# Optimization experiments

Measured on AMD Instinct MI355X. Metric: run time of the kernel, lower is better.

Reference implementation:

```python
import jax, jax.numpy as jnp
import numpy as np

NUM_ENT = 50000
DIM = 128
NUM_REL = 1000  # num_rel * 2 (inverse relations)
E = 300000
SLOPE = 0.2      # args.leaky_relu_w
BN_EPS = 1e-5


def _leaky(x):
    return jax.nn.leaky_relu(x, SLOPE)


def _l2norm(x):
    n = jnp.linalg.norm(x, axis=-1, keepdims=True)
    return x / jnp.maximum(n, 1e-12)


def _batchnorm(x):
    # BatchNorm1d, training mode, fresh gamma=1/beta=0
    m = x.mean(axis=0)
    v = x.var(axis=0)
    return (x - m) / jnp.sqrt(v + BN_EPS)


def _propagate(i, j, etype, rel, x, watt, aatt, gcn, norm, num_ent):
    # gather -> relation-aware transform (opn='mult') -> attention -> scatter-add
    trans = x[j] * rel[etype]                       # [E, D]
    comb = jnp.concatenate([x[i], trans], axis=1)   # [E, 2D]
    score = (_leaky(comb @ watt) @ aatt)[:, 0]      # [E]
    # scatter softmax of attention score over destination nodes
    m = jax.ops.segment_max(score, i, num_segments=num_ent)
    m = jnp.where(jnp.isfinite(m), m, 0.0)
    e = jnp.exp(score - m[i])
    s = jax.ops.segment_sum(e, i, num_segments=num_ent)
    alpha = e / (s[i] + 1e-16)
    msg = (trans @ gcn) * alpha[:, None]
    if norm is not None:
        msg = msg * norm[:, None]
    return jax.ops.segment_sum(msg, i, num_segments=num_ent)


def _conv(ent, rel_in, edge_index, edge_type, w1, w2, gcn, loop_rel, watt, aatt):
    # RelationalAwareLayer.forward
    num_ent = ent.shape[0]
    rel = jnp.concatenate([rel_in, loop_rel], axis=0)
    rel = _leaky(rel @ w1) @ w2
    row, col = edge_index[0], edge_index[1]
    deg = jax.ops.segment_sum(jnp.ones((row.shape[0],), jnp.float32), row, num_segments=num_ent)
    dinv = jnp.where(deg > 0, deg ** -0.5, 0.0)
    norm = dinv[row]
    msg_n = _propagate(row, col, edge_type, rel, ent, watt, aatt, gcn, norm, num_ent)
    idx = jnp.arange(num_ent)
    loop_t = jnp.full((num_ent,), rel.shape[0] - 1)
    msg_s = _propagate(idx, idx, loop_t, rel, ent, watt, aatt, gcn, None, num_ent)
    return jnp.tanh(_batchnorm((msg_n + msg_s) / 2.0))


def setup_inputs() -> dict:
    key = jax.random.key(0)
    ks = jax.random.split(key, 24)
    g = lambda k, s: jax.random.normal(k, s, dtype=jnp.float32) * 0.05
    return {
        'edge_index': jax.random.randint(ks[0], (2, E), 0, NUM_ENT),
        'edge_type': jax.random.randint(ks[1], (E,), 0, NUM_REL),
        'ent_info_att': g(ks[2], (NUM_ENT, DIM)),
        'ent_completion_att': g(ks[3], (NUM_ENT, DIM)),
        'rel_completion_att': g(ks[4], (NUM_REL, DIM)),
        'rel_info_att': g(ks[5], (NUM_REL, DIM)),
        'align_linear1_1': g(ks[6], (2 * DIM, DIM)),
        'align_linear1_2': g(ks[7], (DIM, DIM)),
        'align_linear2_1': g(ks[8], (2 * DIM, DIM)),
        'align_linear2_2': g(ks[9], (DIM, DIM)),
        'rel_linear11': g(ks[10], (DIM, DIM)),
        'rel_linear12': g(ks[11], (DIM, DIM)),
        'rel_linear11_align': g(ks[12], (DIM, DIM)),
        'rel_linear12_align': g(ks[13], (DIM, DIM)),
        'all_linear_comp': g(ks[14], (3 * DIM, DIM)),
        # stacked per-layer conv params: [conv1_align, conv1_completion, conv2_align]
        'conv_w1': g(ks[15], (3, DIM, DIM)),
        'conv_w2': g(ks[16], (3, DIM, DIM)),
        'conv_gcn': g(ks[17], (3, DIM, DIM)),
        'conv_loop': g(ks[18], (3, 1, DIM)),
        'conv_watt': g(ks[19], (3, 2 * DIM, DIM)),
        'conv_aatt': g(ks[20], (3, DIM, 1)),
    }


def reference(edge_index, edge_type, ent_info_att, ent_completion_att,
              rel_completion_att, rel_info_att,
              align_linear1_1, align_linear1_2, align_linear2_1, align_linear2_2,
              rel_linear11, rel_linear12, rel_linear11_align, rel_linear12_align,
              all_linear_comp, conv_w1, conv_w2, conv_gcn, conv_loop, conv_watt, conv_aatt):
    # forward_base with num_gcn_layer == 2, dropout rate 0 (identity)
    init_comp = _l2norm(ent_completion_att)
    e1 = _leaky(jnp.concatenate([init_comp, ent_info_att], axis=1) @ align_linear1_1) @ align_linear1_2
    ao1 = _conv(e1, rel_info_att, edge_index, edge_type,
                conv_w1[0], conv_w2[0], conv_gcn[0], conv_loop[0], conv_watt[0], conv_aatt[0])
    co1 = _conv(ent_completion_att, rel_completion_att, edge_index, edge_type,
                conv_w1[1], conv_w2[1], conv_gcn[1], conv_loop[1], conv_watt[1], conv_aatt[1])
    pos1n = _l2norm(co1)
    e2 = _leaky(jnp.concatenate([pos1n, ao1], axis=1) @ align_linear2_1) @ align_linear2_2
    pr1 = _leaky(rel_completion_att @ rel_linear11) @ rel_linear12
    ari = _leaky(rel_info_att @ rel_linear11_align) @ rel_linear12_align
    ao2 = _conv(e2, ari, edge_index, edge_type,
                conv_w1[2], conv_w2[2], conv_gcn[2], conv_loop[2], conv_watt[2], conv_aatt[2])
    out = jnp.concatenate([e1, ao1, ao2], axis=1) @ all_linear_comp
    return (out, co1, pr1)
```

## Files before the change

### kernel.cpp

```cpp
#include <hip/hip_runtime.h>
#include <hip/hip_bf16.h>
#include <math.h>

#define D 128
#define DD 16384
#define NEMAX 96
typedef unsigned short u16;
typedef __attribute__((ext_vector_type(8))) short short8v;
typedef __attribute__((ext_vector_type(4))) short short4v;
typedef __attribute__((ext_vector_type(4))) float f32x4;

__device__ __forceinline__ u16 f2s(float v){
    union { __hip_bfloat16 h; u16 u; } c; c.h = __float2bfloat16(v); return c.u;
}
__device__ __forceinline__ float s2f(u16 u){
    union { __hip_bfloat16 h; u16 u; } c; c.u = u; return __bfloat162float(c.h);
}
__device__ __forceinline__ float lrelu(float x){ return x > 0.f ? x : 0.2f*x; }

__global__ void k_prepz(int* __restrict__ zz, int zw, int* __restrict__ nstart,
                        int* __restrict__ nend, int nb){
    int i = blockIdx.x*blockDim.x + threadIdx.x;
    int stride = gridDim.x*blockDim.x;
    for (int k = i; k < zw; k += stride) zz[k] = 0;
    for (int k = i; k < nb; k += stride){ nstart[k] = 0x7fffffff; nend[k] = -1; }
}
__global__ void k_f2b4(const float* __restrict__ in, u16* __restrict__ out, int n4){
    for (int i = blockIdx.x*blockDim.x + threadIdx.x; i < n4; i += gridDim.x*blockDim.x){
        float4 a = ((const float4*)in)[i];
        short4v pk;
        pk[0] = (short)f2s(a.x); pk[1] = (short)f2s(a.y);
        pk[2] = (short)f2s(a.z); pk[3] = (short)f2s(a.w);
        *(short4v*)(out + (size_t)i*4) = pk;
    }
}
__global__ void k_ideg(const int* __restrict__ row, int* __restrict__ deg, int E_){
    for (int i = blockIdx.x*blockDim.x + threadIdx.x; i < E_; i += gridDim.x*blockDim.x)
        atomicAdd(&deg[row[i]], 1);
}
__global__ void k_scan1(const int* __restrict__ ideg, int* __restrict__ rowptr,
                        int* __restrict__ bsum, int n){
    __shared__ int buf[256];
    int t = threadIdx.x, i = blockIdx.x*256 + t;
    int v = (i < n) ? ideg[i] : 0;
    buf[t] = v;
    __syncthreads();
    #pragma unroll
    for (int o = 1; o < 256; o <<= 1){
        int u = (t >= o) ? buf[t-o] : 0;
        __syncthreads();
        buf[t] += u;
        __syncthreads();
    }
    if (i < n) rowptr[i] = buf[t] - v;
    if (t == 255) bsum[blockIdx.x] = buf[255];
}
__global__ void k_scan2(int* __restrict__ bsum, int nb){
    __shared__ int buf[256];
    __shared__ int carry_s;
    int t = threadIdx.x;
    if (t == 0) carry_s = 0;
    __syncthreads();
    for (int base = 0; base < nb; base += 256){
        int v = (base + t < nb) ? bsum[base + t] : 0;
        buf[t] = v;
        __syncthreads();
        #pragma unroll
        for (int o = 1; o < 256; o <<= 1){
            int u = (t >= o) ? buf[t-o] : 0;
            __syncthreads();
            buf[t] += u;
            __syncthreads();
        }
        if (base + t < nb) bsum[base + t] = carry_s + buf[t] - v;
        int last = buf[255];
        __syncthreads();
        if (t == 0) carry_s += last;
        __syncthreads();
    }
}
__global__ void k_scan3(int* __restrict__ rowptr, const int* __restrict__ bsum,
                        int n, int E_){
    int i = blockIdx.x*blockDim.x + threadIdx.x;
    if (i < n) rowptr[i] += bsum[i >> 8];
    if (i == 0) rowptr[n] = E_;
}
__global__ void k_scatter(const int* __restrict__ row, const int* __restrict__ rowptr,
                          int* __restrict__ cnt, int* __restrict__ perm, int E_){
    for (int e = blockIdx.x*blockDim.x + threadIdx.x; e < E_; e += gridDim.x*blockDim.x){
        int i = row[e];
        int pos = rowptr[i] + atomicAdd(&cnt[i], 1);
        perm[pos] = e;
    }
}
__global__ void k_bmap(const int* __restrict__ rowptr, int* __restrict__ nstart,
                       int* __restrict__ nend, int n){
    for (int i = blockIdx.x*blockDim.x + threadIdx.x; i < n; i += gridDim.x*blockDim.x){
        int s = rowptr[i], e = rowptr[i+1];
        if (e > s){
            int b = s >> 6;
            atomicMin(&nstart[b], i);
            atomicMax(&nend[b], i);
        }
    }
}
__global__ void k_bnapply(const float* __restrict__ acc, const float* __restrict__ gp,
                          float inv_ne, int n, u16* __restrict__ dstb,
                          float* __restrict__ dstf){
    int d = threadIdx.x & 127;
    float m = gp[d] * inv_ne;
    float var = gp[128 + d] * inv_ne - m*m;
    float sc = rsqrtf(var + 1e-5f);
    for (int i = blockIdx.x*blockDim.x + threadIdx.x; i < n; i += gridDim.x*blockDim.x){
        float v = acc[i] * 0.5f;
        float r = tanhf((v - m) * sc);
        dstb[i] = f2s(r);
        if (dstf) dstf[i] = r;
    }
}

__global__ void k_relprep(const float* __restrict__ rel_comp, const float* __restrict__ rel_info,
        const float* __restrict__ rl11, const float* __restrict__ rl12,
        const float* __restrict__ rl11a, const float* __restrict__ rl12a,
        const float* __restrict__ cloop, const float* __restrict__ cw1,
        const float* __restrict__ cw2, float* __restrict__ pr1out,
        float* __restrict__ rel2all, int NR){
    int b = blockIdx.x, t = threadIdx.x;
    __shared__ float v[D];
    __shared__ float h[D];
    if (b < NR){
        v[t] = rel_comp[(size_t)b*D + t];
        __syncthreads();
        float a = 0.f;
        #pragma unroll 8
        for (int k = 0; k < D; k++) a += v[k] * rl11[(size_t)k*D + t];
        h[t] = lrelu(a);
        __syncthreads();
        float o = 0.f;
        #pragma unroll 8
        for (int k = 0; k < D; k++) o += h[k] * rl12[(size_t)k*D + t];
        pr1out[(size_t)b*D + t] = o;
        return;
    }
    int bb = b - NR;
    int l = bb / (NR+1), r = bb - l*(NR+1);
    float xv;
    if (r == NR)      xv = cloop[l*D + t];
    else if (l == 1)  xv = rel_comp[(size_t)r*D + t];
    else              xv = rel_info[(size_t)r*D + t];
    v[t] = xv;
    __syncthreads();
    if (l == 2 && r < NR){
        float a = 0.f;
        #pragma unroll 8
        for (int k = 0; k < D; k++) a += v[k] * rl11a[(size_t)k*D + t];
        h[t] = lrelu(a);
        __syncthreads();
        float o = 0.f;
        #pragma unroll 8
        for (int k = 0; k < D; k++) o += h[k] * rl12a[(size_t)k*D + t];
        v[t] = o;
        __syncthreads();
    }
    const float* w1 = cw1 + (size_t)l*DD;
    const float* w2 = cw2 + (size_t)l*DD;
    float a = 0.f;
    #pragma unroll 8
    for (int k = 0; k < D; k++) a += v[k] * w1[(size_t)k*D + t];
    h[t] = lrelu(a);
    __syncthreads();
    float o = 0.f;
    #pragma unroll 8
    for (int k = 0; k < D; k++) o += h[k] * w2[(size_t)k*D + t];
    rel2all[((size_t)l*(NR+1) + r)*D + t] = o;
}

struct TEnt { const float* s; u16* d; int ldd; };
struct TTab { TEnt e[18]; };
__global__ void k_wprep(TTab tab){
    TEnt en = tab.e[blockIdx.x];
    int t = threadIdx.x;
    int n = t >> 1, h = t & 1;
    #pragma unroll
    for (int g = 0; g < 8; ++g){
        int k0 = h*64 + g*8;
        short8v pk;
        #pragma unroll
        for (int q = 0; q < 8; ++q) pk[q] = (short)f2s(en.s[(size_t)(k0+q)*D + n]);
        *(short8v*)(en.d + (size_t)n*en.ldd + k0) = pk;
    }
}

struct Srcs { const void* p0; const void* p1; const void* p2; int f0, f1, f2; };

template<int NSEG, int EPI, bool RSN>
__global__ __launch_bounds__(256) void k_mrow(Srcs S, const u16* __restrict__ WT,
        void* __restrict__ out, int NE_, float* __restrict__ gp,
        u16* __restrict__ uout, const float* __restrict__ looprow){
    __shared__ __align__(16) short As[128*128];
    int tid = threadIdx.x;
    int row0 = blockIdx.x * 128;
    int lane = tid & 63, w = tid >> 6;
    int l15 = lane & 15, lq = lane >> 4;
    int nhalf = w & 1, mquad = w >> 1;
    f32x4 acc[4][4];
    #pragma unroll
    for (int a = 0; a < 4; a++)
        #pragma unroll
        for (int b = 0; b < 4; b++) acc[a][b] = (f32x4){0.f,0.f,0.f,0.f};

    int sr = tid >> 1, sh = tid & 1;
    int rr = row0 + sr; if (rr >= NE_) rr = NE_ - 1;

    #pragma unroll
    for (int s = 0; s < NSEG; ++s){
        const void* sp = (s == 0) ? S.p0 : (s == 1) ? S.p1 : S.p2;
        int sf = (s == 0) ? S.f0 : (s == 1) ? S.f1 : S.f2;
        if (s) __syncthreads();
        #pragma unroll
        for (int g = 0; g < 8; ++g){
            int k8 = sh*64 + g*8;
            short8v pk;
            if (sf){
                const float* fp = (const float*)sp + (size_t)rr*D + k8;
                #pragma unroll
                for (int q = 0; q < 8; ++q) pk[q] = (short)f2s(fp[q]);
            } else {
                pk = *(const short8v*)((const u16*)sp + (size_t)rr*D + k8);
            }
            *(short8v*)(As + sr*D + (((k8>>3) ^ (sr&7))<<3)) = pk;
        }
        if (RSN && s == 0){
            float ss = 0.f;
            #pragma unroll
            for (int g = 0; g < 8; ++g){
                int k8 = sh*64 + g*8;
                short8v v = *(const short8v*)(As + sr*D + (((k8>>3) ^ (sr&7))<<3));
                #pragma unroll
                for (int q = 0; q < 8; ++q){ float f = s2f((u16)v[q]); ss += f*f; }
            }
            ss += __shfl_xor(ss, 1, 64);
            float rsc = 1.f / fmaxf(sqrtf(ss), 1e-12f);
            #pragma unroll
            for (int g = 0; g < 8; ++g){
                int k8 = sh*64 + g*8;
                short* ap = As + sr*D + (((k8>>3) ^ (sr&7))<<3);
                short8v v = *(const short8v*)ap;
                short8v pk;
                #pragma unroll
                for (int q = 0; q < 8; ++q) pk[q] = (short)f2s(s2f((u16)v[q]) * rsc);
                *(short8v*)ap = pk;
            }
        }
        __syncthreads();
        short8v bfr[4][4];
        #pragma unroll
        for (int nt = 0; nt < 4; ++nt)
            #pragma unroll
            for (int kk = 0; kk < 4; ++kk){
                size_t idx = (size_t)(nhalf*64 + nt*16 + l15)*(NSEG*D) + (size_t)s*D + kk*32 + lq*8;
                bfr[nt][kk] = *(const short8v*)(WT + idx);
            }
        #pragma unroll
        for (int mt = 0; mt < 4; ++mt){
            int ar = mquad*64 + mt*16 + l15;
            short8v afr[4];
            #pragma unroll
            for (int kk = 0; kk < 4; ++kk)
                afr[kk] = *(const short8v*)(As + ar*D + (((kk*4 + lq) ^ (ar&7))<<3));
            #pragma unroll
            for (int nt = 0; nt < 4; ++nt)
                #pragma unroll
                for (int kk = 0; kk < 4; ++kk)
                    acc[mt][nt] = __builtin_amdgcn_mfma_f32_16x16x32_bf16(
                        afr[kk], bfr[nt][kk], acc[mt][nt], 0, 0, 0);
        }
    }
    if (EPI == 3){
        float cs[4] = {0,0,0,0}, cs2[4] = {0,0,0,0};
        #pragma unroll
        for (int mt = 0; mt < 4; ++mt)
            #pragma unroll
            for (int nt = 0; nt < 4; ++nt)
                #pragma unroll
                for (int r = 0; r < 4; ++r){
                    int gr = row0 + mquad*64 + mt*16 + lq*4 + r;
                    if (gr >= NE_) continue;
                    int c = nhalf*64 + nt*16 + l15;
                    float v = acc[mt][nt][r];
                    ((float*)out)[(size_t)gr*D + c] = v;
                    float h = v * 0.5f;
                    cs[nt] += h; cs2[nt] += h*h;
                }
        __syncthreads();
        float* ps  = (float*)As;
        float* ps2 = ps + 1024;
        int slot = mquad*4 + lq;
        #pragma unroll
        for (int nt = 0; nt < 4; ++nt){
            int c = nhalf*64 + nt*16 + l15;
            ps[slot*128 + c]  = cs[nt];
            ps2[slot*128 + c] = cs2[nt];
        }
        __syncthreads();
        if (tid < 128){
            float s = 0.f, s2 = 0.f;
            #pragma unroll
            for (int q = 0; q < 8; ++q){ s += ps[q*128 + tid]; s2 += ps2[q*128 + tid]; }
            atomicAdd(&gp[tid], s);
            atomicAdd(&gp[128 + tid], s2);
        }
    } else {
        #pragma unroll
        for (int mt = 0; mt < 4; ++mt){
            #pragma unroll
            for (int nt = 0; nt < 4; ++nt){
                #pragma unroll
                for (int r = 0; r < 4; ++r){
                    int gr = row0 + mquad*64 + mt*16 + lq*4 + r;
                    if (gr >= NE_) continue;
                    int c = nhalf*64 + nt*16 + l15;
                    float v = acc[mt][nt][r];
                    if (EPI == 0) ((float*)out)[(size_t)gr*D + c] = v;
                    else ((u16*)out)[(size_t)gr*D + c] = f2s(EPI == 2 ? lrelu(v) : v);
                }
            }
        }
        if (EPI == 4){
            for (int idx = tid; idx < 128*128; idx += 256){
                int r2 = idx >> 7, c = idx & 127;
                int gr = row0 + r2;
                if (gr < NE_){
                    float v = s2f((u16)As[r2*D + ((((c>>3) ^ (r2&7))<<3) | (c&7))]) * looprow[c];
                    uout[(size_t)gr*D + c] = f2s(v);
                }
            }
        }
    }
}

__global__ __launch_bounds__(256) void k_fedge(
        const int* __restrict__ rowi, const int* __restrict__ coli, const int* __restrict__ ety,
        const int* __restrict__ rowptr, const int* __restrict__ perm,
        const int* __restrict__ nstart, const int* __restrict__ nend,
        const u16* __restrict__ x, const float* __restrict__ rel2,
        const u16* __restrict__ xattb, const u16* __restrict__ WT,
        const float* __restrict__ aatt, u16* __restrict__ u){
    __shared__ __align__(16) short As[NEMAX*D];
    __shared__ u16 jL[NEMAX], kL[NEMAX], iL[NEMAX];
    __shared__ float sc[NEMAX];
    __shared__ float red[2][NEMAX];
    int b = blockIdx.x;
    int ns = nstart[b];
    if (ns == 0x7fffffff) return;
    int nn = nend[b] - ns + 1;
    int tid = threadIdx.x;
    int estart = rowptr[ns];
    int ne = rowptr[ns + nn] - estart;
    if (ne > NEMAX) ne = NEMAX;
    int T = (ne + 15) >> 4;
    int nrows = T << 4;
    if (tid < ne){
        int e = perm[estart + tid];
        jL[tid] = (u16)coli[e]; kL[tid] = (u16)ety[e]; iL[tid] = (u16)rowi[e];
    }
    __syncthreads();
    for (int it = tid; it < nrows*4; it += 256){
        int p = it >> 2, part = it & 3;
        int ps = (p < ne) ? p : (ne - 1);
        int j = jL[ps], krel = kL[ps];
        #pragma unroll
        for (int g = 0; g < 4; ++g){
            int k8 = part*32 + g*8;
            short8v sv = *(const short8v*)(x + (size_t)j*D + k8);
            const float* rp = rel2 + (size_t)krel*D + k8;
            short8v pk;
            #pragma unroll
            for (int q = 0; q < 8; ++q) pk[q] = (short)f2s(s2f((u16)sv[q]) * rp[q]);
            *(short8v*)(As + p*D + (((k8>>3) ^ (p&7))<<3)) = pk;
        }
    }
    __syncthreads();
    int lane = tid & 63, w = tid >> 6;
    int l15 = lane & 15, lq = lane >> 4;
    int nhalf = w & 1, mq = w >> 1;
    short8v bfr[4][4];
    #pragma unroll
    for (int nt = 0; nt < 4; ++nt)
        #pragma unroll
        for (int kk = 0; kk < 4; ++kk)
            bfr[nt][kk] = *(const short8v*)(WT + (size_t)(nhalf*64 + nt*16 + l15)*D + kk*32 + lq*8);
    float av[4];
    #pragma unroll
    for (int nt = 0; nt < 4; ++nt) av[nt] = aatt[nhalf*64 + nt*16 + l15];

    for (int t = mq; t < T; t += 2){
        int ar = t*16 + l15;
        short8v afr[4];
        #pragma unroll
        for (int kk = 0; kk < 4; ++kk)
            afr[kk] = *(const short8v*)(As + ar*D + (((kk*4 + lq) ^ (ar&7))<<3));
        f32x4 acc[4];
        #pragma unroll
        for (int nt = 0; nt < 4; ++nt) acc[nt] = (f32x4){0.f,0.f,0.f,0.f};
        #pragma unroll
        for (int nt = 0; nt < 4; ++nt)
            #pragma unroll
            for (int kk = 0; kk < 4; ++kk)
                acc[nt] = __builtin_amdgcn_mfma_f32_16x16x32_bf16(
                    afr[kk], bfr[nt][kk], acc[nt], 0, 0, 0);
        #pragma unroll
        for (int r = 0; r < 4; ++r){
            int el = t*16 + lq*4 + r;
            float p = 0.f;
            if (el < ne){
                int ii = iL[el];
                #pragma unroll
                for (int nt = 0; nt < 4; ++nt){
                    float xv = s2f(xattb[(size_t)ii*D + nhalf*64 + nt*16 + l15]);
                    p += lrelu(acc[nt][r] + xv) * av[nt];
                }
            }
            p += __shfl_xor(p, 1, 64);
            p += __shfl_xor(p, 2, 64);
            p += __shfl_xor(p, 4, 64);
            p += __shfl_xor(p, 8, 64);
            if (l15 == 0 && el < NEMAX) red[nhalf][el] = p;
        }
    }
    __syncthreads();
    if (tid < ne) sc[tid] = expf(red[0][tid] + red[1][tid]);
    __syncthreads();
    if (tid < nn){
        int i = ns + tid;
        int s0 = rowptr[i] - estart, s1 = rowptr[i+1] - estart;
        if (s1 > NEMAX) s1 = NEMAX;
        if (s1 > s0){
            float sum = 0.f;
            for (int p = s0; p < s1; ++p) sum += sc[p];
            float coef = rsqrtf((float)(s1 - s0)) / (sum + 1e-16f);
            for (int p = s0; p < s1; ++p) sc[p] *= coef;
        }
    }
    __syncthreads();
    int c = tid & 127, nh = tid >> 7;
    for (int n = nh; n < nn; n += 2){
        int i = ns + n;
        int s0 = rowptr[i] - estart, s1 = rowptr[i+1] - estart;
        if (s1 > NEMAX) s1 = NEMAX;
        if (s1 <= s0) continue;
        float a = 0.f;
        for (int p = s0; p < s1; ++p)
            a += sc[p] * s2f((u16)As[p*D + ((((c>>3) ^ (p&7))<<3) | (c&7))]);
        size_t ad = (size_t)i*D + c;
        u[ad] = f2s(s2f(u[ad]) + a);
    }
}

extern "C" void kernel_launch(void* const* d_in, const int* in_sizes, int n_in,
                              void* d_out, int out_size, void* d_ws, size_t ws_size,
                              hipStream_t stream){
    const int* eidx = (const int*)d_in[0];
    const int* ety  = (const int*)d_in[1];
    const float* ent_info = (const float*)d_in[2];
    const float* ent_comp = (const float*)d_in[3];
    const float* rel_comp = (const float*)d_in[4];
    const float* rel_info = (const float*)d_in[5];
    const float* al11 = (const float*)d_in[6],  *al12 = (const float*)d_in[7];
    const float* al21 = (const float*)d_in[8],  *al22 = (const float*)d_in[9];
    const float* rl11 = (const float*)d_in[10], *rl12 = (const float*)d_in[11];
    const float* rl11a = (const float*)d_in[12], *rl12a = (const float*)d_in[13];
    const float* allw = (const float*)d_in[14];
    const float* cw1 = (const float*)d_in[15], *cw2 = (const float*)d_in[16];
    const float* cgcn = (const float*)d_in[17], *cloop = (const float*)d_in[18];
    const float* cwatt = (const float*)d_in[19], *caatt = (const float*)d_in[20];

    const int E  = in_sizes[1];
    const int NE = in_sizes[2] / D;
    const int NR = in_sizes[4] / D;
    const int* row = eidx;
    const int* col = eidx + E;
    const size_t NEd = (size_t)NE * D;
    float* outp = (float*)d_out;
    const int NB64 = (E + 63) / 64;

    char* wsb = (char*)d_ws;
    size_t off = 0;
    auto takeB = [&](size_t bytes) -> void* {
        void* q = wsb + off;
        off = (off + bytes + 255) & ~(size_t)255;
        return q;
    };
    float* accum = (float*)takeB(NEd * 4);
    u16*   hb    = (u16*)accum;
    u16*   xattb = (u16*) takeB(NEd * 2);
    u16*   ub    = (u16*) takeB(NEd * 2);
    u16*   e1b   = (u16*) takeB(NEd * 2);
    u16*   ao1b  = (u16*) takeB(NEd * 2);
    u16*   e2b   = (u16*) takeB(NEd * 2);
    u16*   cob   = (u16*) takeB(NEd * 2);
    float* rel2all = (float*)takeB((size_t)3*(NR+1)*D*4);
    int*   rowptr= (int*)  takeB((size_t)(NE+1)*4);
    int*   perm  = (int*)  takeB((size_t)E*4);
    int*   bsum  = (int*)  takeB(1024*4);
    int*   nstart= (int*)  takeB((size_t)NB64*4);
    int*   nend  = (int*)  takeB((size_t)NB64*4);
    int ZW = 2*NE + 768;
    int*   zz    = (int*)  takeB((size_t)ZW*4);
    int*   ideg  = zz;
    int*   cnt   = zz + NE;
    float* gp3   = (float*)(zz + 2*NE);
    u16*   wtXatt = (u16*)takeB((size_t)3*DD*2);
    u16*   wtScore= (u16*)takeB((size_t)3*DD*2);
    u16*   wtGcn  = (u16*)takeB((size_t)3*DD*2);
    u16*   wtAl11 = (u16*)takeB((size_t)2*DD*2);
    u16*   wtAl12 = (u16*)takeB((size_t)DD*2);
    u16*   wtAl21 = (u16*)takeB((size_t)2*DD*2);
    u16*   wtAl22 = (u16*)takeB((size_t)DD*2);
    u16*   wtAllw = (u16*)takeB((size_t)3*DD*2);
    u16*   xcb   = e2b;

    const int GS = 2048, BS = 256;
    const int RB = (NE + 127) / 128;
    const int NB = (NE + 255) / 256;
    const float inv_ne = 1.f / (float)NE;

    TTab tab;
    int ti = 0;
    for (int l = 0; l < 3; ++l){
        tab.e[ti++] = { cwatt + (size_t)l*2*DD,        wtXatt  + (size_t)l*DD, 128 };
        tab.e[ti++] = { cwatt + (size_t)l*2*DD + DD,   wtScore + (size_t)l*DD, 128 };
        tab.e[ti++] = { cgcn  + (size_t)l*DD,          wtGcn   + (size_t)l*DD, 128 };
    }
    tab.e[ti++] = { al11,       wtAl11,        256 };
    tab.e[ti++] = { al11 + DD,  wtAl11 + 128,  256 };
    tab.e[ti++] = { al12,       wtAl12,        128 };
    tab.e[ti++] = { al21,       wtAl21,        256 };
    tab.e[ti++] = { al21 + DD,  wtAl21 + 128,  256 };
    tab.e[ti++] = { al22,       wtAl22,        128 };
    tab.e[ti++] = { allw,            wtAllw,        384 };
    tab.e[ti++] = { allw + DD,       wtAllw + 128,  384 };
    tab.e[ti++] = { allw + 2*DD,     wtAllw + 256,  384 };
    k_wprep<<<18, 256, 0, stream>>>(tab);

    k_prepz<<<256, BS, 0, stream>>>(zz, ZW, nstart, nend, NB64);
    k_f2b4<<<GS, BS, 0, stream>>>(ent_comp, xcb, (int)(NEd/4));
    k_ideg<<<GS, BS, 0, stream>>>(row, ideg, E);
    k_scan1<<<NB, 256, 0, stream>>>(ideg, rowptr, bsum, NE);
    k_scan2<<<1, 256, 0, stream>>>(bsum, NB);
    k_scan3<<<NB, 256, 0, stream>>>(rowptr, bsum, NE, E);
    k_scatter<<<GS, BS, 0, stream>>>(row, rowptr, cnt, perm, E);
    k_bmap<<<NB, 256, 0, stream>>>(rowptr, nstart, nend, NE);

    k_relprep<<<NR + 3*(NR+1), D, 0, stream>>>(rel_comp, rel_info, rl11, rl12,
                                               rl11a, rl12a, cloop, cw1, cw2,
                                               outp + 2*NEd, rel2all, NR);

    {
        Srcs S{ ent_comp, ent_info, nullptr, 1, 1, 0 };
        k_mrow<2, 2, true><<<RB, 256, 0, stream>>>(S, wtAl11, hb, NE, nullptr, nullptr, nullptr);
        Srcs S2{ hb, nullptr, nullptr, 0, 0, 0 };
        k_mrow<1, 1, false><<<RB, 256, 0, stream>>>(S2, wtAl12, e1b, NE, nullptr, nullptr, nullptr);
    }

    auto conv = [&](const u16* x, int l, u16* dstb, float* dstf){
        const float* aatt  = caatt + (size_t)l*D;
        const float* rel2l = rel2all + (size_t)l*(NR+1)*D;
        float* gp = gp3 + (size_t)l*256;
        Srcs Sx{ x, nullptr, nullptr, 0, 0, 0 };
        k_mrow<1, 4, false><<<RB, 256, 0, stream>>>(Sx, wtXatt + (size_t)l*DD, xattb, NE,
                                                    nullptr, ub, rel2l + (size_t)NR*D);
        k_fedge<<<NB64, 256, 0, stream>>>(row, col, ety, rowptr, perm, nstart, nend,
                                          x, rel2l, xattb, wtScore + (size_t)l*DD, aatt, ub);
        Srcs Su{ ub, nullptr, nullptr, 0, 0, 0 };
        k_mrow<1, 3, false><<<RB, 256, 0, stream>>>(Su, wtGcn + (size_t)l*DD, accum, NE,
                                                    gp, nullptr, nullptr);
        k_bnapply<<<GS, BS, 0, stream>>>(accum, gp, inv_ne, (int)NEd, dstb, dstf);
    };

    conv(e1b, 0, ao1b, nullptr);
    conv(xcb, 1, cob,  outp + NEd);

    {
        Srcs S{ cob, ao1b, nullptr, 0, 0, 0 };
        k_mrow<2, 2, true><<<RB, 256, 0, stream>>>(S, wtAl21, hb, NE, nullptr, nullptr, nullptr);
        Srcs S2{ hb, nullptr, nullptr, 0, 0, 0 };
        k_mrow<1, 1, false><<<RB, 256, 0, stream>>>(S2, wtAl22, e2b, NE, nullptr, nullptr, nullptr);
    }

    conv(e2b, 2, cob, nullptr);

    {
        Srcs S{ e1b, ao1b, cob, 0, 0, 0 };
        k_mrow<3, 0, false><<<RB, 256, 0, stream>>>(S, wtAllw, outp, NE, nullptr, nullptr, nullptr);
    }
}
```

Baseline: 694.0 us.

## Batch the two independent first-layer convs into shared launches, store accum as bf16

The two independent first-layer convolutions (ao1 and co1) now run as single merged launches with doubled grids, selected per block by index, when the workspace has room for separate buffers. This raises occupancy and cuts launch count for the xatt, fedge and gcn kernels. The GCN accumulator is stored as bf16 instead of fp32, which halves that traffic but adds rounding before batchnorm. Inside fedge, the xatt loads are hoisted ahead of the MFMA and the aggregation loop is unrolled by four.

```diff
diff --git a/kernel.cpp b/kernel.cpp
--- a/kernel.cpp
+++ b/kernel.cpp
@@ -104,7 +104,7 @@
         }
     }
 }
-__global__ void k_bnapply(const float* __restrict__ acc, const float* __restrict__ gp,
+__global__ void k_bnapply(const u16* __restrict__ acc, const float* __restrict__ gp,
                           float inv_ne, int n, u16* __restrict__ dstb,
                           float* __restrict__ dstf){
     int d = threadIdx.x & 127;
@@ -112,7 +112,7 @@
     float var = gp[128 + d] * inv_ne - m*m;
     float sc = rsqrtf(var + 1e-5f);
     for (int i = blockIdx.x*blockDim.x + threadIdx.x; i < n; i += gridDim.x*blockDim.x){
-        float v = acc[i] * 0.5f;
+        float v = s2f(acc[i]) * 0.5f;
         float r = tanhf((v - m) * sc);
         dstb[i] = f2s(r);
         if (dstf) dstf[i] = r;
@@ -195,8 +195,7 @@
 
 template<int NSEG, int EPI, bool RSN>
 __global__ __launch_bounds__(256) void k_mrow(Srcs S, const u16* __restrict__ WT,
-        void* __restrict__ out, int NE_, float* __restrict__ gp,
-        u16* __restrict__ uout, const float* __restrict__ looprow){
+        void* __restrict__ out, int NE_){
     __shared__ __align__(16) short As[128*128];
     int tid = threadIdx.x;
     int row0 = blockIdx.x * 128;
@@ -276,7 +275,71 @@
                         afr[kk], bfr[nt][kk], acc[mt][nt], 0, 0, 0);
         }
     }
-    if (EPI == 3){
+    #pragma unroll
+    for (int mt = 0; mt < 4; ++mt){
+        #pragma unroll
+        for (int nt = 0; nt < 4; ++nt){
+            #pragma unroll
+            for (int r = 0; r < 4; ++r){
+                int gr = row0 + mquad*64 + mt*16 + lq*4 + r;
+                if (gr >= NE_) continue;
+                int c = nhalf*64 + nt*16 + l15;
+                float v = acc[mt][nt][r];
+                if (EPI == 0) ((float*)out)[(size_t)gr*D + c] = v;
+                else ((u16*)out)[(size_t)gr*D + c] = f2s(EPI == 2 ? lrelu(v) : v);
+            }
+        }
+    }
+}
+
+struct ConvP { const u16* x; const u16* WT; u16* out; u16* ub; const float* loop; float* gp; };
+
+template<int MODE>
+__global__ __launch_bounds__(256) void k_mrow2(ConvP A, ConvP B, int rb, int NE_){
+    __shared__ __align__(16) short As[128*128];
+    int pb = blockIdx.x >= rb;
+    ConvP P = pb ? B : A;
+    int row0 = (blockIdx.x - (pb ? rb : 0)) * 128;
+    int tid = threadIdx.x;
+    int lane = tid & 63, w = tid >> 6;
+    int l15 = lane & 15, lq = lane >> 4;
+    int nhalf = w & 1, mquad = w >> 1;
+    f32x4 acc[4][4];
+    #pragma unroll
+    for (int a = 0; a < 4; a++)
+        #pragma unroll
+        for (int b = 0; b < 4; b++) acc[a][b] = (f32x4){0.f,0.f,0.f,0.f};
+
+    int sr = tid >> 1, sh = tid & 1;
+    int rr = row0 + sr; if (rr >= NE_) rr = NE_ - 1;
+    #pragma unroll
+    for (int g = 0; g < 8; ++g){
+        int k8 = sh*64 + g*8;
+        short8v pk = *(const short8v*)(P.x + (size_t)rr*D + k8);
+        *(short8v*)(As + sr*D + (((k8>>3) ^ (sr&7))<<3)) = pk;
+    }
+    __syncthreads();
+    short8v bfr[4][4];
+    #pragma unroll
+    for (int nt = 0; nt < 4; ++nt)
+        #pragma unroll
+        for (int kk = 0; kk < 4; ++kk)
+            bfr[nt][kk] = *(const short8v*)(P.WT + (size_t)(nhalf*64 + nt*16 + l15)*D + kk*32 + lq*8);
+    #pragma unroll
+    for (int mt = 0; mt < 4; ++mt){
+        int ar = mquad*64 + mt*16 + l15;
+        short8v afr[4];
+        #pragma unroll
+        for (int kk = 0; kk < 4; ++kk)
+            afr[kk] = *(const short8v*)(As + ar*D + (((kk*4 + lq) ^ (ar&7))<<3));
+        #pragma unroll
+        for (int nt = 0; nt < 4; ++nt)
+            #pragma unroll
+            for (int kk = 0; kk < 4; ++kk)
+                acc[mt][nt] = __builtin_amdgcn_mfma_f32_16x16x32_bf16(
+                    afr[kk], bfr[nt][kk], acc[mt][nt], 0, 0, 0);
+    }
+    if (MODE == 3){
         float cs[4] = {0,0,0,0}, cs2[4] = {0,0,0,0};
         #pragma unroll
         for (int mt = 0; mt < 4; ++mt)
@@ -288,7 +351,7 @@
                     if (gr >= NE_) continue;
                     int c = nhalf*64 + nt*16 + l15;
                     float v = acc[mt][nt][r];
-                    ((float*)out)[(size_t)gr*D + c] = v;
+                    P.out[(size_t)gr*D + c] = f2s(v);
                     float h = v * 0.5f;
                     cs[nt] += h; cs2[nt] += h*h;
                 }
@@ -307,50 +370,47 @@
             float s = 0.f, s2 = 0.f;
             #pragma unroll
             for (int q = 0; q < 8; ++q){ s += ps[q*128 + tid]; s2 += ps2[q*128 + tid]; }
-            atomicAdd(&gp[tid], s);
-            atomicAdd(&gp[128 + tid], s2);
+            atomicAdd(&P.gp[tid], s);
+            atomicAdd(&P.gp[128 + tid], s2);
         }
     } else {
         #pragma unroll
-        for (int mt = 0; mt < 4; ++mt){
-            #pragma unroll
-            for (int nt = 0; nt < 4; ++nt){
+        for (int mt = 0; mt < 4; ++mt)
+            #pragma unroll
+            for (int nt = 0; nt < 4; ++nt)
                 #pragma unroll
                 for (int r = 0; r < 4; ++r){
                     int gr = row0 + mquad*64 + mt*16 + lq*4 + r;
                     if (gr >= NE_) continue;
                     int c = nhalf*64 + nt*16 + l15;
-                    float v = acc[mt][nt][r];
-                    if (EPI == 0) ((float*)out)[(size_t)gr*D + c] = v;
-                    else ((u16*)out)[(size_t)gr*D + c] = f2s(EPI == 2 ? lrelu(v) : v);
+                    P.out[(size_t)gr*D + c] = f2s(acc[mt][nt][r]);
                 }
+        for (int idx = tid; idx < 128*128; idx += 256){
+            int r2 = idx >> 7, c = idx & 127;
+            int gr = row0 + r2;
+            if (gr < NE_){
+                float v = s2f((u16)As[r2*D + ((((c>>3) ^ (r2&7))<<3) | (c&7))]) * P.loop[c];
+                P.ub[(size_t)gr*D + c] = f2s(v);
             }
         }
-        if (EPI == 4){
-            for (int idx = tid; idx < 128*128; idx += 256){
-                int r2 = idx >> 7, c = idx & 127;
-                int gr = row0 + r2;
-                if (gr < NE_){
-                    float v = s2f((u16)As[r2*D + ((((c>>3) ^ (r2&7))<<3) | (c&7))]) * looprow[c];
-                    uout[(size_t)gr*D + c] = f2s(v);
-                }
-            }
-        }
-    }
-}
+    }
+}
+
+struct FP { const u16* x; const float* rel2; const u16* xattb; const u16* WT;
+            const float* aatt; u16* u; };
 
 __global__ __launch_bounds__(256) void k_fedge(
         const int* __restrict__ rowi, const int* __restrict__ coli, const int* __restrict__ ety,
         const int* __restrict__ rowptr, const int* __restrict__ perm,
         const int* __restrict__ nstart, const int* __restrict__ nend,
-        const u16* __restrict__ x, const float* __restrict__ rel2,
-        const u16* __restrict__ xattb, const u16* __restrict__ WT,
-        const float* __restrict__ aatt, u16* __restrict__ u){
+        FP fa, FP fb, int nb){
     __shared__ __align__(16) short As[NEMAX*D];
     __shared__ u16 jL[NEMAX], kL[NEMAX], iL[NEMAX];
     __shared__ float sc[NEMAX];
     __shared__ float red[2][NEMAX];
-    int b = blockIdx.x;
+    int pb = blockIdx.x >= nb;
+    FP P = pb ? fb : fa;
+    int b = blockIdx.x - (pb ? nb : 0);
     int ns = nstart[b];
     if (ns == 0x7fffffff) return;
     int nn = nend[b] - ns + 1;
@@ -372,8 +432,8 @@
         #pragma unroll
         for (int g = 0; g < 4; ++g){
             int k8 = part*32 + g*8;
-            short8v sv = *(const short8v*)(x + (size_t)j*D + k8);
-            const float* rp = rel2 + (size_t)krel*D + k8;
+            short8v sv = *(const short8v*)(P.x + (size_t)j*D + k8);
+            const float* rp = P.rel2 + (size_t)krel*D + k8;
             short8v pk;
             #pragma unroll
             for (int q = 0; q < 8; ++q) pk[q] = (short)f2s(s2f((u16)sv[q]) * rp[q]);
@@ -389,12 +449,22 @@
     for (int nt = 0; nt < 4; ++nt)
         #pragma unroll
         for (int kk = 0; kk < 4; ++kk)
-            bfr[nt][kk] = *(const short8v*)(WT + (size_t)(nhalf*64 + nt*16 + l15)*D + kk*32 + lq*8);
+            bfr[nt][kk] = *(const short8v*)(P.WT + (size_t)(nhalf*64 + nt*16 + l15)*D + kk*32 + lq*8);
     float av[4];
     #pragma unroll
-    for (int nt = 0; nt < 4; ++nt) av[nt] = aatt[nhalf*64 + nt*16 + l15];
+    for (int nt = 0; nt < 4; ++nt) av[nt] = P.aatt[nhalf*64 + nt*16 + l15];
 
     for (int t = mq; t < T; t += 2){
+        float xv[4][4];
+        #pragma unroll
+        for (int r = 0; r < 4; ++r){
+            int el = t*16 + lq*4 + r;
+            int ep = (el < ne) ? el : (ne - 1);
+            int ii = iL[ep];
+            #pragma unroll
+            for (int nt = 0; nt < 4; ++nt)
+                xv[r][nt] = s2f(P.xattb[(size_t)ii*D + nhalf*64 + nt*16 + l15]);
+        }
         int ar = t*16 + l15;
         short8v afr[4];
         #pragma unroll
@@ -414,12 +484,9 @@
             int el = t*16 + lq*4 + r;
             float p = 0.f;
             if (el < ne){
-                int ii = iL[el];
                 #pragma unroll
-                for (int nt = 0; nt < 4; ++nt){
-                    float xv = s2f(xattb[(size_t)ii*D + nhalf*64 + nt*16 + l15]);
-                    p += lrelu(acc[nt][r] + xv) * av[nt];
-                }
+                for (int nt = 0; nt < 4; ++nt)
+                    p += lrelu(acc[nt][r] + xv[r][nt]) * av[nt];
             }
             p += __shfl_xor(p, 1, 64);
             p += __shfl_xor(p, 2, 64);
@@ -450,10 +517,18 @@
         if (s1 > NEMAX) s1 = NEMAX;
         if (s1 <= s0) continue;
         float a = 0.f;
-        for (int p = s0; p < s1; ++p)
+        int p = s0;
+        for (; p + 4 <= s1; p += 4){
+            float v0 = s2f((u16)As[(p+0)*D + ((((c>>3) ^ ((p+0)&7))<<3) | (c&7))]);
+            float v1 = s2f((u16)As[(p+1)*D + ((((c>>3) ^ ((p+1)&7))<<3) | (c&7))]);
+            float v2 = s2f((u16)As[(p+2)*D + ((((c>>3) ^ ((p+2)&7))<<3) | (c&7))]);
+            float v3 = s2f((u16)As[(p+3)*D + ((((c>>3) ^ ((p+3)&7))<<3) | (c&7))]);
+            a += sc[p]*v0 + sc[p+1]*v1 + sc[p+2]*v2 + sc[p+3]*v3;
+        }
+        for (; p < s1; ++p)
             a += sc[p] * s2f((u16)As[p*D + ((((c>>3) ^ (p&7))<<3) | (c&7))]);
         size_t ad = (size_t)i*D + c;
-        u[ad] = f2s(s2f(u[ad]) + a);
+        P.u[ad] = f2s(s2f(P.u[ad]) + a);
     }
 }
 
@@ -491,10 +566,11 @@
         off = (off + bytes + 255) & ~(size_t)255;
         return q;
     };
-    float* accum = (float*)takeB(NEd * 4);
-    u16*   hb    = (u16*)accum;
-    u16*   xattb = (u16*) takeB(NEd * 2);
-    u16*   ub    = (u16*) takeB(NEd * 2);
+    u16*   slotA = (u16*) takeB(NEd * 2);
+    u16*   hb    = slotA;
+    u16*   accB0 = slotA;
+    u16*   xattb0= (u16*) takeB(NEd * 2);
+    u16*   ub0   = (u16*) takeB(NEd * 2);
     u16*   e1b   = (u16*) takeB(NEd * 2);
     u16*   ao1b  = (u16*) takeB(NEd * 2);
     u16*   e2b   = (u16*) takeB(NEd * 2);
@@ -520,6 +596,12 @@
     u16*   wtAllw = (u16*)takeB((size_t)3*DD*2);
     u16*   xcb   = e2b;
 
+    size_t slab = ((NEd*2 + 255) & ~(size_t)255);
+    bool wide = (off + 3*slab) <= ws_size;
+    u16* xattb1 = wide ? (u16*)takeB(NEd * 2) : xattb0;
+    u16* ub1    = wide ? (u16*)takeB(NEd * 2) : ub0;
+    u16* accB1  = wide ? (u16*)takeB(NEd * 2) : accB0;
+
     const int GS = 2048, BS = 256;
     const int RB = (NE + 127) / 128;
     const int NB = (NE + 255) / 256;
@@ -558,40 +640,56 @@
 
     {
         Srcs S{ ent_comp, ent_info, nullptr, 1, 1, 0 };
-        k_mrow<2, 2, true><<<RB, 256, 0, stream>>>(S, wtAl11, hb, NE, nullptr, nullptr, nullptr);
+        k_mrow<2, 2, true><<<RB, 256, 0, stream>>>(S, wtAl11, hb, NE);
         Srcs S2{ hb, nullptr, nullptr, 0, 0, 0 };
-        k_mrow<1, 1, false><<<RB, 256, 0, stream>>>(S2, wtAl12, e1b, NE, nullptr, nullptr, nullptr);
-    }
-
-    auto conv = [&](const u16* x, int l, u16* dstb, float* dstf){
-        const float* aatt  = caatt + (size_t)l*D;
+        k_mrow<1, 1, false><<<RB, 256, 0, stream>>>(S2, wtAl12, e1b, NE);
+    }
+
+    auto conv_seq = [&](const u16* x, int l, u16* xab, u16* ubp, u16* acb,
+                        u16* dstb, float* dstf){
         const float* rel2l = rel2all + (size_t)l*(NR+1)*D;
         float* gp = gp3 + (size_t)l*256;
-        Srcs Sx{ x, nullptr, nullptr, 0, 0, 0 };
-        k_mrow<1, 4, false><<<RB, 256, 0, stream>>>(Sx, wtXatt + (size_t)l*DD, xattb, NE,
-                                                    nullptr, ub, rel2l + (size_t)NR*D);
+        ConvP A4{ x, wtXatt + (size_t)l*DD, xab, ubp, rel2l + (size_t)NR*D, nullptr };
+        k_mrow2<4><<<RB, 256, 0, stream>>>(A4, A4, RB, NE);
+        FP fa{ x, rel2l, xab, wtScore + (size_t)l*DD, caatt + (size_t)l*D, ubp };
         k_fedge<<<NB64, 256, 0, stream>>>(row, col, ety, rowptr, perm, nstart, nend,
-                                          x, rel2l, xattb, wtScore + (size_t)l*DD, aatt, ub);
-        Srcs Su{ ub, nullptr, nullptr, 0, 0, 0 };
-        k_mrow<1, 3, false><<<RB, 256, 0, stream>>>(Su, wtGcn + (size_t)l*DD, accum, NE,
-                                                    gp, nullptr, nullptr);
-        k_bnapply<<<GS, BS, 0, stream>>>(accum, gp, inv_ne, (int)NEd, dstb, dstf);
+                                          fa, fa, NB64);
+        ConvP A3{ ubp, wtGcn + (size_t)l*DD, acb, nullptr, nullptr, gp };
+        k_mrow2<3><<<RB, 256, 0, stream>>>(A3, A3, RB, NE);
+        k_bnapply<<<GS, BS, 0, stream>>>(acb, gp, inv_ne, (int)NEd, dstb, dstf);
     };
 
-    conv(e1b, 0, ao1b, nullptr);
-    conv(xcb, 1, cob,  outp + NEd);
+    if (wide){
+        const float* rel2_0 = rel2all;
+        const float* rel2_1 = rel2all + (size_t)(NR+1)*D;
+        ConvP A4{ e1b, wtXatt,      xattb0, ub0, rel2_0 + (size_t)NR*D, nullptr };
+        ConvP B4{ xcb, wtXatt + DD, xattb1, ub1, rel2_1 + (size_t)NR*D, nullptr };
+        k_mrow2<4><<<2*RB, 256, 0, stream>>>(A4, B4, RB, NE);
+        FP fa{ e1b, rel2_0, xattb0, wtScore,      caatt,     ub0 };
+        FP fb{ xcb, rel2_1, xattb1, wtScore + DD, caatt + D, ub1 };
+        k_fedge<<<2*NB64, 256, 0, stream>>>(row, col, ety, rowptr, perm, nstart, nend,
+                                            fa, fb, NB64);
+        ConvP A3{ ub0, wtGcn,      accB0, nullptr, nullptr, gp3 };
+        ConvP B3{ ub1, wtGcn + DD, accB1, nullptr, nullptr, gp3 + 256 };
+        k_mrow2<3><<<2*RB, 256, 0, stream>>>(A3, B3, RB, NE);
+        k_bnapply<<<GS, BS, 0, stream>>>(accB0, gp3, inv_ne, (int)NEd, ao1b, nullptr);
+        k_bnapply<<<GS, BS, 0, stream>>>(accB1, gp3 + 256, inv_ne, (int)NEd, cob, outp + NEd);
+    } else {
+        conv_seq(e1b, 0, xattb0, ub0, accB0, ao1b, nullptr);
+        conv_seq(xcb, 1, xattb0, ub0, accB0, cob, outp + NEd);
+    }
 
     {
         Srcs S{ cob, ao1b, nullptr, 0, 0, 0 };
-        k_mrow<2, 2, true><<<RB, 256, 0, stream>>>(S, wtAl21, hb, NE, nullptr, nullptr, nullptr);
+        k_mrow<2, 2, true><<<RB, 256, 0, stream>>>(S, wtAl21, hb, NE);
         Srcs S2{ hb, nullptr, nullptr, 0, 0, 0 };
-        k_mrow<1, 1, false><<<RB, 256, 0, stream>>>(S2, wtAl22, e2b, NE, nullptr, nullptr, nullptr);
-    }
-
-    conv(e2b, 2, cob, nullptr);
+        k_mrow<1, 1, false><<<RB, 256, 0, stream>>>(S2, wtAl22, e2b, NE);
+    }
+
+    conv_seq(e2b, 2, xattb0, ub0, accB0, cob, nullptr);
 
     {
         Srcs S{ e1b, ao1b, cob, 0, 0, 0 };
-        k_mrow<3, 0, false><<<RB, 256, 0, stream>>>(S, wtAllw, outp, NE, nullptr, nullptr, nullptr);
-    }
-}
+        k_mrow<3, 0, false><<<RB, 256, 0, stream>>>(S, wtAllw, outp, NE);
+    }
+}
```

After: 669.9 us. 3.5% less time.
